# Kernel optimization log

Hardware: AMD Instinct MI355X
Metric: run time of the kernel (lower is better)

The kernel has to match this reference:

```python
import jax, jax.numpy as jnp
import numpy as np

# norse-default LIF/LI constants (RecNet overrides alpha=80, tau_mem_inv=100)
DT = 0.001
ALPHA = 80.0
TAU_SYN_INV = 200.0   # 1/5e-3 (default)
TAU_MEM_INV = 100.0   # 1/0.01 (passed explicitly)
V_TH, V_RESET, V_LEAK = 1.0, 0.0, 0.0

@jax.custom_vjp
def superspike(x):
    # heaviside forward, SuperSpike surrogate backward
    return (x > 0).astype(x.dtype)

def _ss_fwd(x):
    return (x > 0).astype(x.dtype), x

def _ss_bwd(x, g):
    return (g / (ALPHA * jnp.abs(x) + 1.0) ** 2,)

superspike.defvjp(_ss_fwd, _ss_bwd)

def setup_inputs() -> dict:
    key = jax.random.key(0)
    k1, k2, k3, k4 = jax.random.split(key, 4)
    T, B, F, H, O = 100, 512, 784, 512, 10
    x = jax.random.normal(k1, (T, B, 1, 28, 28), dtype=jnp.float32)
    w_in = jax.random.normal(k2, (H, F), dtype=jnp.float32) / np.sqrt(F)
    w_rec = jax.random.normal(k3, (H, H), dtype=jnp.float32) / np.sqrt(H)
    w_out = jax.random.normal(k4, (O, H), dtype=jnp.float32) / np.sqrt(H)
    return {"x": x, "w_in": w_in, "w_rec": w_rec, "w_out": w_out}

def reference(x, w_in, w_rec, w_out):
    T, B = x.shape[0], x.shape[1]
    Hd = w_in.shape[0]
    Od = w_out.shape[0]
    xf = x.reshape(T, B, -1)  # [T, B, F]

    z0 = jnp.zeros((B, Hd), x.dtype)
    lv0 = jnp.zeros((B, Od), x.dtype)
    init = (z0, z0, z0, lv0, lv0)  # (z, v, i, li_v, li_i)

    def step(carry, xt):
        z, v, i, lv, li = carry
        # LIF recurrent cell (norse lif_step)
        v_dec = v + DT * TAU_MEM_INV * ((V_LEAK - v) + i)
        i_dec = i - DT * TAU_SYN_INV * i
        z_new = superspike(v_dec - V_TH)
        v_new = (1.0 - z_new) * v_dec + z_new * V_RESET
        i_new = i_dec + xt @ w_in.T + z @ w_rec.T  # previous z for recurrence
        # readout linear (no bias)
        y = z_new @ w_out.T
        # LI cell (norse li_feed_forward_step): vo uses old current
        lv_new = lv + DT * TAU_MEM_INV * ((V_LEAK - lv) + li)
        li_new = li - DT * TAU_SYN_INV * li + y
        return (z_new, v_new, i_new, lv_new, li_new), lv_new

    _, voltages = jax.lax.scan(step, init, xf)
    return voltages  # [T, B, O]
```

## Files before the change

kernel.cpp:

```cpp
#include <hip/hip_runtime.h>


#define TT    100
#define BATCH 512
#define FDIM  784
#define HDIM  512
#define ODIM  10
#define NSTATE (BATCH * HDIM)

#define DTM 0.1
#define DTS 0.2

typedef double f64x4 __attribute__((ext_vector_type(4)));

__device__ __forceinline__ void h_maps(int H, int lane,
                                       int& am, int& ak, int& bn, int& bk,
                                       int dr[4], int dc[4]) {
  const int l15 = lane & 15, l4 = lane >> 4;
  const int lq = lane >> 2, l3 = lane & 3;
  if (H & 1) { am = lq;  ak = l3; } else { am = l15; ak = l4; }
  if (H & 2) { bn = lq;  bk = l3; } else { bn = l15; bk = l4; }
  const int dmode = H >> 2;
#pragma unroll
  for (int r = 0; r < 4; ++r) {
    const int rr = (dmode & 1) ? (l4 + (r << 2)) : ((l4 << 2) + r);
    if (dmode & 2) { dr[r] = l15; dc[r] = rr; }
    else           { dr[r] = rr;  dc[r] = l15; }
  }
}

__global__ __launch_bounds__(64) void probe_kernel(int* __restrict__ flag) {
  const int lane = threadIdx.x;
  int winner = -1;
  for (int H = 0; H < 16; ++H) {
    int am, ak, bn, bk, dr[4], dc[4];
    h_maps(H, lane, am, ak, bn, bk, dr, dc);
    bool ok = true;
#pragma unroll
    for (int s = 0; s < 2; ++s) {
      const int c0 = s ? 2 : 3, c1 = s ? 13 : 7, c2 = s ? 9 : 5, c3 = s ? 4 : 11;
      const double a = (double)(1 + c0 * am + c1 * ak);
      const double b = (double)(1 + c2 * bn + c3 * bk);
      f64x4 d = {0.0, 0.0, 0.0, 0.0};
      d = __builtin_amdgcn_mfma_f64_16x16x4f64(a, b, d, 0, 0, 0);
#pragma unroll
      for (int r = 0; r < 4; ++r) {
        double ref = 0.0;
#pragma unroll
        for (int k = 0; k < 4; ++k)
          ref += (double)((1 + c0 * dr[r] + c1 * k) * (1 + c2 * dc[r] + c3 * k));
        ok = ok && (d[r] == ref);
      }
    }
    if (__all(ok) && winner < 0) winner = H;
  }
  if (lane == 0) *flag = winner;
}

__global__ __launch_bounds__(256) void gemm_in_kernel(const float* __restrict__ A,
                                                      const float* __restrict__ B,
                                                      double* __restrict__ C,
                                                      const int* __restrict__ flag) {
  __shared__ __align__(16) double Al[4][16][16];
  __shared__ __align__(16) double Bl[4][16][16];
  const int tid  = threadIdx.x;
  const int lane = tid & 63;
  const int qm   = (tid >> 6) & 1;
  const int qn   = tid >> 7;
  const int n0 = blockIdx.x << 6;
  const int m0 = blockIdx.y << 6;
  const int srow = tid >> 2;
  const int skc  = (tid & 3) << 2;
  const int st = srow >> 4, sr = srow & 15;
  const int H = flag[0];

  const float* Arow = A + (size_t)(m0 + srow) * FDIM + skc;
  const float* Brow = B + (size_t)(n0 + srow) * FDIM + skc;

  if (H >= 0) {
    int am, ak, bn, bk, dr[4], dc[4];
    h_maps(H, lane, am, ak, bn, bk, dr, dc);
    f64x4 acc[2][2] = {};
    for (int kt = 0; kt < 49; ++kt) {
      __syncthreads();
      const float4 a4 = *(const float4*)(Arow + kt * 16);
      Al[st][skc + 0][sr] = (double)a4.x;
      Al[st][skc + 1][sr] = (double)a4.y;
      Al[st][skc + 2][sr] = (double)a4.z;
      Al[st][skc + 3][sr] = (double)a4.w;
      const float4 b4 = *(const float4*)(Brow + kt * 16);
      Bl[st][skc + 0][sr] = (double)b4.x;
      Bl[st][skc + 1][sr] = (double)b4.y;
      Bl[st][skc + 2][sr] = (double)b4.z;
      Bl[st][skc + 3][sr] = (double)b4.w;
      __syncthreads();
#pragma unroll
      for (int ks = 0; ks < 4; ++ks) {
        const double a0 = Al[(qm << 1) + 0][(ks << 2) + ak][am];
        const double a1 = Al[(qm << 1) + 1][(ks << 2) + ak][am];
        const double b0 = Bl[(qn << 1) + 0][(ks << 2) + bk][bn];
        const double b1 = Bl[(qn << 1) + 1][(ks << 2) + bk][bn];
        acc[0][0] = __builtin_amdgcn_mfma_f64_16x16x4f64(a0, b0, acc[0][0], 0, 0, 0);
        acc[0][1] = __builtin_amdgcn_mfma_f64_16x16x4f64(a0, b1, acc[0][1], 0, 0, 0);
        acc[1][0] = __builtin_amdgcn_mfma_f64_16x16x4f64(a1, b0, acc[1][0], 0, 0, 0);
        acc[1][1] = __builtin_amdgcn_mfma_f64_16x16x4f64(a1, b1, acc[1][1], 0, 0, 0);
      }
    }
#pragma unroll
    for (int i = 0; i < 2; ++i)
#pragma unroll
      for (int j = 0; j < 2; ++j)
#pragma unroll
        for (int r = 0; r < 4; ++r)
          C[(size_t)(m0 + (((qm << 1) + i) << 4) + dr[r]) * HDIM
            + n0 + (((qn << 1) + j) << 4) + dc[r]] = acc[i][j][r];
  } else {
    float* Asf = (float*)&Al[0][0][0];
    float* Bsf = (float*)&Bl[0][0][0];
    const int tn = tid & 15, tm = tid >> 4;
    const int lrow = tid >> 2, lkc = (tid & 3) << 2;
    double acc[4][4] = {};
    for (int kt = 0; kt < 49; ++kt) {
      __syncthreads();
      const float4 a = *(const float4*)(A + (size_t)(m0 + lrow) * FDIM + kt * 16 + lkc);
      Asf[(lkc + 0) * 68 + lrow] = a.x; Asf[(lkc + 1) * 68 + lrow] = a.y;
      Asf[(lkc + 2) * 68 + lrow] = a.z; Asf[(lkc + 3) * 68 + lrow] = a.w;
      const float4 b = *(const float4*)(B + (size_t)(n0 + lrow) * FDIM + kt * 16 + lkc);
      Bsf[(lkc + 0) * 68 + lrow] = b.x; Bsf[(lkc + 1) * 68 + lrow] = b.y;
      Bsf[(lkc + 2) * 68 + lrow] = b.z; Bsf[(lkc + 3) * 68 + lrow] = b.w;
      __syncthreads();
#pragma unroll
      for (int kk = 0; kk < 16; ++kk) {
        const float4 af = *(const float4*)&Asf[kk * 68 + (tm << 2)];
        const float4 bf = *(const float4*)&Bsf[kk * 68 + (tn << 2)];
        const double amv[4] = {(double)af.x, (double)af.y, (double)af.z, (double)af.w};
        const double bnv[4] = {(double)bf.x, (double)bf.y, (double)bf.z, (double)bf.w};
#pragma unroll
        for (int i = 0; i < 4; ++i)
#pragma unroll
          for (int j = 0; j < 4; ++j) acc[i][j] += amv[i] * bnv[j];
      }
    }
#pragma unroll
    for (int i = 0; i < 4; ++i) {
      double* crow = C + (size_t)(m0 + (tm << 2) + i) * HDIM + n0 + (tn << 2);
      *(double2*)(crow)     = make_double2(acc[i][0], acc[i][1]);
      *(double2*)(crow + 2) = make_double2(acc[i][2], acc[i][3]);
    }
  }
}

__global__ __launch_bounds__(256) void transpose_kernel(const float* __restrict__ src,
                                                        float* __restrict__ dst) {
  __shared__ float tile[32][33];
  const int bx = blockIdx.x & 15, by = blockIdx.x >> 4;
  const int tx = threadIdx.x & 31, ty = threadIdx.x >> 5;
  const int x = (bx << 5) + tx;
#pragma unroll
  for (int s = 0; s < 32; s += 8)
    tile[ty + s][tx] = src[(size_t)((by << 5) + ty + s) * HDIM + x];
  __syncthreads();
  const int xo = (by << 5) + tx;
#pragma unroll
  for (int s = 0; s < 32; s += 8)
    dst[(size_t)((bx << 5) + ty + s) * HDIM + xo] = tile[tx][ty + s];
}

__global__ __launch_bounds__(256) void wot_kernel(const float* __restrict__ w_out,
                                                  float* __restrict__ wot) {
  const int k = (blockIdx.x << 8) + threadIdx.x;
#pragma unroll
  for (int o = 0; o < ODIM; ++o) wot[(k << 4) + o] = w_out[(size_t)o * HDIM + k];
}

__global__ __launch_bounds__(256) void lif_kernel(const double* __restrict__ cin,
                                                  const float* __restrict__ wrt,
                                                  const float* __restrict__ wot,
                                                  float* __restrict__ out) {
  const int b = blockIdx.x;
  const int tid = threadIdx.x;
  const int h0 = tid, h1 = tid + 256;

  __shared__ unsigned long long masks[8];
  __shared__ int offs[9];
  __shared__ __align__(8) unsigned short list[528];
  __shared__ double ypart[256];

  if (tid == 0) offs[8] = 0;
  __syncthreads();

  double v0 = 0.0, v1 = 0.0, i0 = 0.0, i1 = 0.0;
  double lv = 0.0, li = 0.0;

  const double* cinb = cin + (size_t)b * HDIM;
  float* outb = out + (size_t)b * ODIM;

  for (int t = 0; t < TT; ++t) {
    const double vd0 = v0 + DTM * ((0.0 - v0) + i0);
    const double vd1 = v1 + DTM * ((0.0 - v1) + i1);
    const bool s0 = (vd0 - 1.0) > 0.0;
    const bool s1 = (vd1 - 1.0) > 0.0;
    v0 = s0 ? 0.0 : vd0;
    v1 = s1 ? 0.0 : vd1;
    i0 = i0 - DTS * i0;
    i1 = i1 - DTS * i1;

    const double c0 = cinb[(size_t)t * NSTATE + h0];
    const double c1 = cinb[(size_t)t * NSTATE + h1];

    {
      const int nf = offs[8];
      const int nfp = (nf + 3) & ~3;
      if (nfp > 0) {
        float A0[4], A1[4], B0[4] = {}, B1[4] = {};
#define LOADG(base, X0, X1)                                                   \
        do {                                                                  \
          const unsigned long long le = *(const unsigned long long*)&list[base]; \
          const int k0 = (int)(le & 0xffffu), k1 = (int)((le >> 16) & 0xffffu); \
          const int k2 = (int)((le >> 32) & 0xffffu), k3 = (int)(le >> 48);   \
          X0[0] = wrt[(k0 << 9) + h0]; X1[0] = wrt[(k0 << 9) + h1];           \
          X0[1] = wrt[(k1 << 9) + h0]; X1[1] = wrt[(k1 << 9) + h1];           \
          X0[2] = wrt[(k2 << 9) + h0]; X1[2] = wrt[(k2 << 9) + h1];           \
          X0[3] = wrt[(k3 << 9) + h0]; X1[3] = wrt[(k3 << 9) + h1];           \
        } while (0)
        LOADG(0, A0, A1);
        for (int g = 0; g < nfp; g += 4) {
          if (g + 4 < nfp) LOADG(g + 4, B0, B1);
          i0 += (double)A0[0]; i1 += (double)A1[0];
          i0 += (double)A0[1]; i1 += (double)A1[1];
          i0 += (double)A0[2]; i1 += (double)A1[2];
          i0 += (double)A0[3]; i1 += (double)A1[3];
#pragma unroll
          for (int j = 0; j < 4; ++j) { A0[j] = B0[j]; A1[j] = B1[j]; }
        }
#undef LOADG
      }
    }
    i0 += c0;
    i1 += c1;

    __syncthreads();

    {
      const unsigned long long m0 = __ballot(s0);
      const unsigned long long m1 = __ballot(s1);
      const int w = tid >> 6;
      if ((tid & 63) == 0) { masks[w] = m0; masks[4 + w] = m1; }
    }
    __syncthreads();
    if (tid == 0) {
      int r = 0;
#pragma unroll
      for (int q = 0; q < 8; ++q) { offs[q] = r; r += __popcll(masks[q]); }
      offs[8] = r;
    }
    __syncthreads();
    if (tid < 8) {
      unsigned long long m = masks[tid];
      int o = offs[tid];
      const int base = tid << 6;
      while (m) {
        list[o++] = (unsigned short)(base + __builtin_ctzll(m));
        m &= m - 1;
      }
    }
    if (tid < 4) list[offs[8] + tid] = 512;
    __syncthreads();

    {
      const int o = tid & 15, q = tid >> 4;
      const int nfc = offs[8];
      double yp = 0.0;
      int kk = q;
      if (kk < nfc) {
        float f = wot[((int)list[kk] << 4) + o];
        for (kk += 16; kk < nfc; kk += 16) {
          const float fn = wot[((int)list[kk] << 4) + o];
          yp += (double)f;
          f = fn;
        }
        yp += (double)f;
      }
      ypart[(o << 4) + q] = yp;
    }
    __syncthreads();
    if (tid < ODIM) {
      double y = 0.0;
      const double* yr = &ypart[tid << 4];
#pragma unroll
      for (int q = 0; q < 16; ++q) y += yr[q];
      const double lvn = lv + DTM * ((0.0 - lv) + li);
      li = (li - DTS * li) + y;
      lv = lvn;
      outb[(size_t)t * (BATCH * ODIM) + tid] = (float)lvn;
    }
  }
}

extern "C" void kernel_launch(void* const* d_in, const int* in_sizes, int n_in,
                              void* d_out, int out_size, void* d_ws, size_t ws_size,
                              hipStream_t stream) {
  const float* x     = (const float*)d_in[0];
  const float* w_in  = (const float*)d_in[1];
  const float* w_rec = (const float*)d_in[2];
  const float* w_out = (const float*)d_in[3];
  float* out = (float*)d_out;

  const size_t CIN = (size_t)TT * BATCH * HDIM;
  double* cin = (double*)d_ws;
  float* wrt = (float*)(cin + CIN);
  float* wot = wrt + 513 * 512;
  int* flag  = (int*)(wot + 513 * 16);

  const size_t aux_floats = 513ull * 512 + 513ull * 16;
  const size_t need_bytes = CIN * sizeof(double) + aux_floats * sizeof(float) + 16;
  if (ws_size < need_bytes) {
    hipMemsetAsync(d_out, 0x7F, (size_t)out_size * sizeof(float), stream);
    return;
  }

  hipMemsetAsync(wrt, 0, aux_floats * sizeof(float), stream);
  probe_kernel<<<1, 64, 0, stream>>>(flag);
  transpose_kernel<<<256, 256, 0, stream>>>(w_rec, wrt);
  wot_kernel<<<2, 256, 0, stream>>>(w_out, wot);
  gemm_in_kernel<<<dim3(8, 800), 256, 0, stream>>>(x, w_in, cin, flag);
  lif_kernel<<<BATCH, 256, 0, stream>>>(cin, wrt, wot, out);
}
```

Baseline: 1.192 ms.

## Enlarge input GEMM tile to 128x128 with double-buffered LDS prefetch

The fp64 MFMA input-projection GEMM now uses 128x128 output tiles per block, with a 4x4 fragment grid per wave instead of 2x2, so each loaded A/B element is reused more. It also double-buffers the LDS stage: the next k-slice is fetched into registers while MFMAs run on the current buffer, leaving one barrier per iteration. The aim is to cut global and LDS traffic per flop and to hide load latency. The cost is more accumulator registers (64 doubles per thread) and a smaller grid, which may lower occupancy. The fallback path loops over four 64x64 sub-tiles to match.

```diff
diff --git a/kernel.cpp b/kernel.cpp
--- a/kernel.cpp
+++ b/kernel.cpp
@@ -10,6 +10,8 @@
 
 #define DTM 0.1
 #define DTS 0.2
+
+#define LP 130
 
 typedef double f64x4 __attribute__((ext_vector_type(4)));
 
@@ -61,91 +63,125 @@
                                                       const float* __restrict__ B,
                                                       double* __restrict__ C,
                                                       const int* __restrict__ flag) {
-  __shared__ __align__(16) double Al[4][16][16];
-  __shared__ __align__(16) double Bl[4][16][16];
+  __shared__ __align__(16) double Al[2][16][LP];
+  __shared__ __align__(16) double Bl[2][16][LP];
   const int tid  = threadIdx.x;
   const int lane = tid & 63;
   const int qm   = (tid >> 6) & 1;
   const int qn   = tid >> 7;
-  const int n0 = blockIdx.x << 6;
-  const int m0 = blockIdx.y << 6;
-  const int srow = tid >> 2;
-  const int skc  = (tid & 3) << 2;
-  const int st = srow >> 4, sr = srow & 15;
+  const int n0 = blockIdx.x << 7;
+  const int m0 = blockIdx.y << 7;
   const int H = flag[0];
 
-  const float* Arow = A + (size_t)(m0 + srow) * FDIM + skc;
-  const float* Brow = B + (size_t)(n0 + srow) * FDIM + skc;
+  const int srow0 = tid >> 2;
+  const int skc   = (tid & 3) << 2;
+
+  const float* Arow0 = A + (size_t)(m0 + srow0) * FDIM + skc;
+  const float* Arow1 = Arow0 + (size_t)64 * FDIM;
+  const float* Brow0 = B + (size_t)(n0 + srow0) * FDIM + skc;
+  const float* Brow1 = Brow0 + (size_t)64 * FDIM;
 
   if (H >= 0) {
     int am, ak, bn, bk, dr[4], dc[4];
     h_maps(H, lane, am, ak, bn, bk, dr, dc);
-    f64x4 acc[2][2] = {};
+    f64x4 acc[4][4] = {};
+
+#define STAGE(bf, va0, va1, vb0, vb1)                                   \
+    do {                                                                \
+      _Pragma("unroll")                                                 \
+      for (int j = 0; j < 4; ++j) {                                     \
+        Al[bf][skc + j][srow0]      = (double)(&(va0).x)[j];            \
+        Al[bf][skc + j][srow0 + 64] = (double)(&(va1).x)[j];            \
+        Bl[bf][skc + j][srow0]      = (double)(&(vb0).x)[j];            \
+        Bl[bf][skc + j][srow0 + 64] = (double)(&(vb1).x)[j];            \
+      }                                                                 \
+    } while (0)
+
+    {
+      const float4 a0 = *(const float4*)(Arow0);
+      const float4 a1 = *(const float4*)(Arow1);
+      const float4 b0 = *(const float4*)(Brow0);
+      const float4 b1 = *(const float4*)(Brow1);
+      STAGE(0, a0, a1, b0, b1);
+    }
+    __syncthreads();
+
+    int cur = 0;
     for (int kt = 0; kt < 49; ++kt) {
+      float4 na0, na1, nb0, nb1;
+      if (kt < 48) {
+        na0 = *(const float4*)(Arow0 + (kt + 1) * 16);
+        na1 = *(const float4*)(Arow1 + (kt + 1) * 16);
+        nb0 = *(const float4*)(Brow0 + (kt + 1) * 16);
+        nb1 = *(const float4*)(Brow1 + (kt + 1) * 16);
+      }
+#pragma unroll
+      for (int ks = 0; ks < 4; ++ks) {
+        double fa[4], fb[4];
+#pragma unroll
+        for (int mf = 0; mf < 4; ++mf)
+          fa[mf] = Al[cur][(ks << 2) + ak][(qm << 6) + (mf << 4) + am];
+#pragma unroll
+        for (int nf = 0; nf < 4; ++nf)
+          fb[nf] = Bl[cur][(ks << 2) + bk][(qn << 6) + (nf << 4) + bn];
+#pragma unroll
+        for (int mf = 0; mf < 4; ++mf)
+#pragma unroll
+          for (int nf = 0; nf < 4; ++nf)
+            acc[mf][nf] = __builtin_amdgcn_mfma_f64_16x16x4f64(fa[mf], fb[nf],
+                                                               acc[mf][nf], 0, 0, 0);
+      }
+      if (kt < 48) STAGE(cur ^ 1, na0, na1, nb0, nb1);
       __syncthreads();
-      const float4 a4 = *(const float4*)(Arow + kt * 16);
-      Al[st][skc + 0][sr] = (double)a4.x;
-      Al[st][skc + 1][sr] = (double)a4.y;
-      Al[st][skc + 2][sr] = (double)a4.z;
-      Al[st][skc + 3][sr] = (double)a4.w;
-      const float4 b4 = *(const float4*)(Brow + kt * 16);
-      Bl[st][skc + 0][sr] = (double)b4.x;
-      Bl[st][skc + 1][sr] = (double)b4.y;
-      Bl[st][skc + 2][sr] = (double)b4.z;
-      Bl[st][skc + 3][sr] = (double)b4.w;
-      __syncthreads();
-#pragma unroll
-      for (int ks = 0; ks < 4; ++ks) {
-        const double a0 = Al[(qm << 1) + 0][(ks << 2) + ak][am];
-        const double a1 = Al[(qm << 1) + 1][(ks << 2) + ak][am];
-        const double b0 = Bl[(qn << 1) + 0][(ks << 2) + bk][bn];
-        const double b1 = Bl[(qn << 1) + 1][(ks << 2) + bk][bn];
-        acc[0][0] = __builtin_amdgcn_mfma_f64_16x16x4f64(a0, b0, acc[0][0], 0, 0, 0);
-        acc[0][1] = __builtin_amdgcn_mfma_f64_16x16x4f64(a0, b1, acc[0][1], 0, 0, 0);
-        acc[1][0] = __builtin_amdgcn_mfma_f64_16x16x4f64(a1, b0, acc[1][0], 0, 0, 0);
-        acc[1][1] = __builtin_amdgcn_mfma_f64_16x16x4f64(a1, b1, acc[1][1], 0, 0, 0);
-      }
-    }
-#pragma unroll
-    for (int i = 0; i < 2; ++i)
-#pragma unroll
-      for (int j = 0; j < 2; ++j)
+      cur ^= 1;
+    }
+#undef STAGE
+
+#pragma unroll
+    for (int mf = 0; mf < 4; ++mf)
+#pragma unroll
+      for (int nf = 0; nf < 4; ++nf)
 #pragma unroll
         for (int r = 0; r < 4; ++r)
-          C[(size_t)(m0 + (((qm << 1) + i) << 4) + dr[r]) * HDIM
-            + n0 + (((qn << 1) + j) << 4) + dc[r]] = acc[i][j][r];
+          C[(size_t)(m0 + (qm << 6) + (mf << 4) + dr[r]) * HDIM
+            + n0 + (qn << 6) + (nf << 4) + dc[r]] = acc[mf][nf][r];
   } else {
     float* Asf = (float*)&Al[0][0][0];
     float* Bsf = (float*)&Bl[0][0][0];
     const int tn = tid & 15, tm = tid >> 4;
     const int lrow = tid >> 2, lkc = (tid & 3) << 2;
-    double acc[4][4] = {};
-    for (int kt = 0; kt < 49; ++kt) {
+    for (int sub = 0; sub < 4; ++sub) {
+      const int sm0 = m0 + ((sub & 1) << 6);
+      const int sn0 = n0 + ((sub >> 1) << 6);
+      double acc[4][4] = {};
+      for (int kt = 0; kt < 49; ++kt) {
+        __syncthreads();
+        const float4 a = *(const float4*)(A + (size_t)(sm0 + lrow) * FDIM + kt * 16 + lkc);
+        Asf[(lkc + 0) * 68 + lrow] = a.x; Asf[(lkc + 1) * 68 + lrow] = a.y;
+        Asf[(lkc + 2) * 68 + lrow] = a.z; Asf[(lkc + 3) * 68 + lrow] = a.w;
+        const float4 b = *(const float4*)(B + (size_t)(sn0 + lrow) * FDIM + kt * 16 + lkc);
+        Bsf[(lkc + 0) * 68 + lrow] = b.x; Bsf[(lkc + 1) * 68 + lrow] = b.y;
+        Bsf[(lkc + 2) * 68 + lrow] = b.z; Bsf[(lkc + 3) * 68 + lrow] = b.w;
+        __syncthreads();
+#pragma unroll
+        for (int kk = 0; kk < 16; ++kk) {
+          const float4 af = *(const float4*)&Asf[kk * 68 + (tm << 2)];
+          const float4 bf = *(const float4*)&Bsf[kk * 68 + (tn << 2)];
+          const double amv[4] = {(double)af.x, (double)af.y, (double)af.z, (double)af.w};
+          const double bnv[4] = {(double)bf.x, (double)bf.y, (double)bf.z, (double)bf.w};
+#pragma unroll
+          for (int i = 0; i < 4; ++i)
+#pragma unroll
+            for (int j = 0; j < 4; ++j) acc[i][j] += amv[i] * bnv[j];
+        }
+      }
+#pragma unroll
+      for (int i = 0; i < 4; ++i) {
+        double* crow = C + (size_t)(sm0 + (tm << 2) + i) * HDIM + sn0 + (tn << 2);
+        *(double2*)(crow)     = make_double2(acc[i][0], acc[i][1]);
+        *(double2*)(crow + 2) = make_double2(acc[i][2], acc[i][3]);
+      }
       __syncthreads();
-      const float4 a = *(const float4*)(A + (size_t)(m0 + lrow) * FDIM + kt * 16 + lkc);
-      Asf[(lkc + 0) * 68 + lrow] = a.x; Asf[(lkc + 1) * 68 + lrow] = a.y;
-      Asf[(lkc + 2) * 68 + lrow] = a.z; Asf[(lkc + 3) * 68 + lrow] = a.w;
-      const float4 b = *(const float4*)(B + (size_t)(n0 + lrow) * FDIM + kt * 16 + lkc);
-      Bsf[(lkc + 0) * 68 + lrow] = b.x; Bsf[(lkc + 1) * 68 + lrow] = b.y;
-      Bsf[(lkc + 2) * 68 + lrow] = b.z; Bsf[(lkc + 3) * 68 + lrow] = b.w;
-      __syncthreads();
-#pragma unroll
-      for (int kk = 0; kk < 16; ++kk) {
-        const float4 af = *(const float4*)&Asf[kk * 68 + (tm << 2)];
-        const float4 bf = *(const float4*)&Bsf[kk * 68 + (tn << 2)];
-        const double amv[4] = {(double)af.x, (double)af.y, (double)af.z, (double)af.w};
-        const double bnv[4] = {(double)bf.x, (double)bf.y, (double)bf.z, (double)bf.w};
-#pragma unroll
-        for (int i = 0; i < 4; ++i)
-#pragma unroll
-          for (int j = 0; j < 4; ++j) acc[i][j] += amv[i] * bnv[j];
-      }
-    }
-#pragma unroll
-    for (int i = 0; i < 4; ++i) {
-      double* crow = C + (size_t)(m0 + (tm << 2) + i) * HDIM + n0 + (tn << 2);
-      *(double2*)(crow)     = make_double2(acc[i][0], acc[i][1]);
-      *(double2*)(crow + 2) = make_double2(acc[i][2], acc[i][3]);
     }
   }
 }
@@ -323,6 +359,6 @@
   probe_kernel<<<1, 64, 0, stream>>>(flag);
   transpose_kernel<<<256, 256, 0, stream>>>(w_rec, wrt);
   wot_kernel<<<2, 256, 0, stream>>>(w_out, wot);
-  gemm_in_kernel<<<dim3(8, 800), 256, 0, stream>>>(x, w_in, cin, flag);
+  gemm_in_kernel<<<dim3(4, 400), 256, 0, stream>>>(x, w_in, cin, flag);
   lif_kernel<<<BATCH, 256, 0, stream>>>(cin, wrt, wot, out);
 }
```

After: 1.320 ms. 10.8% more time.

## Split input GEMM rows between FP64 MFMA blocks and VALU FMA blocks

Applied to the files above, without the earlier changes.

The input-projection GEMM now runs as a 1D grid where each period of 37 blocks mixes 24 MFMA-tiled blocks (64x64 tiles, first 24576 rows) and 13 VALU-FMA blocks (128x64 tiles, remaining 26624 rows). The aim is to use the FP64 matrix cores and the vector ALUs at the same time, so the GEMM is no longer limited by matrix-core throughput alone. Interleaving the two block types keeps both kinds resident on each CU. The risk is an imbalance between the two paths, and the larger shared-memory footprint may reduce occupancy.

```diff
diff --git a/kernel.cpp b/kernel.cpp
--- a/kernel.cpp
+++ b/kernel.cpp
@@ -10,6 +10,10 @@
 
 #define DTM 0.1
 #define DTS 0.2
+
+#define M_MFMA_BLKS 3072
+#define M_VALU_BLKS 1664
+#define PERIOD 37
 
 typedef double f64x4 __attribute__((ext_vector_type(4)));
 
@@ -61,25 +65,29 @@
                                                       const float* __restrict__ B,
                                                       double* __restrict__ C,
                                                       const int* __restrict__ flag) {
-  __shared__ __align__(16) double Al[4][16][16];
-  __shared__ __align__(16) double Bl[4][16][16];
-  const int tid  = threadIdx.x;
-  const int lane = tid & 63;
-  const int qm   = (tid >> 6) & 1;
-  const int qn   = tid >> 7;
-  const int n0 = blockIdx.x << 6;
-  const int m0 = blockIdx.y << 6;
-  const int srow = tid >> 2;
-  const int skc  = (tid & 3) << 2;
-  const int st = srow >> 4, sr = srow & 15;
+  __shared__ __align__(16) char smem[25088];
+  const int tid = threadIdx.x;
+  const int id = blockIdx.x;
+  const int p = id / PERIOD, r = id % PERIOD;
+  const bool is_mfma_blk = (r < 24);
   const int H = flag[0];
 
-  const float* Arow = A + (size_t)(m0 + srow) * FDIM + skc;
-  const float* Brow = B + (size_t)(n0 + srow) * FDIM + skc;
-
-  if (H >= 0) {
+  if (is_mfma_blk && H >= 0) {
+    const int mb = p * 24 + r;
+    const int n0 = (mb & 7) << 6;
+    const int m0 = (mb >> 3) << 6;
+    double (*Al)[16][16] = (double(*)[16][16])smem;
+    double (*Bl)[16][16] = (double(*)[16][16])(smem + 8192);
+    const int lane = tid & 63;
+    const int qm = (tid >> 6) & 1;
+    const int qn = tid >> 7;
+    const int srow = tid >> 2;
+    const int skc  = (tid & 3) << 2;
+    const int st = srow >> 4, sr = srow & 15;
     int am, ak, bn, bk, dr[4], dc[4];
     h_maps(H, lane, am, ak, bn, bk, dr, dc);
+    const float* Arow = A + (size_t)(m0 + srow) * FDIM + skc;
+    const float* Brow = B + (size_t)(n0 + srow) * FDIM + skc;
     f64x4 acc[2][2] = {};
     for (int kt = 0; kt < 49; ++kt) {
       __syncthreads();
@@ -111,12 +119,15 @@
 #pragma unroll
       for (int j = 0; j < 2; ++j)
 #pragma unroll
-        for (int r = 0; r < 4; ++r)
-          C[(size_t)(m0 + (((qm << 1) + i) << 4) + dr[r]) * HDIM
-            + n0 + (((qn << 1) + j) << 4) + dc[r]] = acc[i][j][r];
-  } else {
-    float* Asf = (float*)&Al[0][0][0];
-    float* Bsf = (float*)&Bl[0][0][0];
+        for (int rr = 0; rr < 4; ++rr)
+          C[(size_t)(m0 + (((qm << 1) + i) << 4) + dr[rr]) * HDIM
+            + n0 + (((qn << 1) + j) << 4) + dc[rr]] = acc[i][j][rr];
+  } else if (is_mfma_blk) {
+    const int mb = p * 24 + r;
+    const int n0 = (mb & 7) << 6;
+    const int m0 = (mb >> 3) << 6;
+    float* Asf = (float*)smem;
+    float* Bsf = (float*)(smem + 4352);
     const int tn = tid & 15, tm = tid >> 4;
     const int lrow = tid >> 2, lkc = (tid & 3) << 2;
     double acc[4][4] = {};
@@ -144,6 +155,55 @@
 #pragma unroll
     for (int i = 0; i < 4; ++i) {
       double* crow = C + (size_t)(m0 + (tm << 2) + i) * HDIM + n0 + (tn << 2);
+      *(double2*)(crow)     = make_double2(acc[i][0], acc[i][1]);
+      *(double2*)(crow + 2) = make_double2(acc[i][2], acc[i][3]);
+    }
+  } else {
+    const int vb = p * 13 + (r - 24);
+    const int n0 = (vb & 7) << 6;
+    const int m0 = 24576 + ((vb >> 3) << 7);
+    double (*As)[130] = (double(*)[130])smem;
+    double (*Bs)[66]  = (double(*)[66])(smem + 16640);
+    const int tn = tid & 15;
+    const int tm = tid >> 4;
+    double acc[8][4] = {};
+    for (int kt = 0; kt < 49; ++kt) {
+      __syncthreads();
+#pragma unroll
+      for (int s = 0; s < 2; ++s) {
+        const int idx = tid + (s << 8);
+        const int row = idx >> 2;
+        const int kc  = (idx & 3) << 2;
+        const float4 a = *(const float4*)(A + (size_t)(m0 + row) * FDIM + kt * 16 + kc);
+        As[kc + 0][row] = (double)a.x; As[kc + 1][row] = (double)a.y;
+        As[kc + 2][row] = (double)a.z; As[kc + 3][row] = (double)a.w;
+      }
+      {
+        const int row = tid >> 2;
+        const int kc  = (tid & 3) << 2;
+        const float4 b = *(const float4*)(B + (size_t)(n0 + row) * FDIM + kt * 16 + kc);
+        Bs[kc + 0][row] = (double)b.x; Bs[kc + 1][row] = (double)b.y;
+        Bs[kc + 2][row] = (double)b.z; Bs[kc + 3][row] = (double)b.w;
+      }
+      __syncthreads();
+#pragma unroll
+      for (int kk = 0; kk < 16; ++kk) {
+        double av[8], bv[4];
+        *(double2*)&av[0] = *(const double2*)&As[kk][(tm << 3) + 0];
+        *(double2*)&av[2] = *(const double2*)&As[kk][(tm << 3) + 2];
+        *(double2*)&av[4] = *(const double2*)&As[kk][(tm << 3) + 4];
+        *(double2*)&av[6] = *(const double2*)&As[kk][(tm << 3) + 6];
+        *(double2*)&bv[0] = *(const double2*)&Bs[kk][(tn << 2) + 0];
+        *(double2*)&bv[2] = *(const double2*)&Bs[kk][(tn << 2) + 2];
+#pragma unroll
+        for (int i = 0; i < 8; ++i)
+#pragma unroll
+          for (int j = 0; j < 4; ++j) acc[i][j] += av[i] * bv[j];
+      }
+    }
+#pragma unroll
+    for (int i = 0; i < 8; ++i) {
+      double* crow = C + (size_t)(m0 + (tm << 3) + i) * HDIM + n0 + (tn << 2);
       *(double2*)(crow)     = make_double2(acc[i][0], acc[i][1]);
       *(double2*)(crow + 2) = make_double2(acc[i][2], acc[i][3]);
     }
@@ -249,10 +309,10 @@
     }
     __syncthreads();
     if (tid == 0) {
-      int r = 0;
-#pragma unroll
-      for (int q = 0; q < 8; ++q) { offs[q] = r; r += __popcll(masks[q]); }
-      offs[8] = r;
+      int rr = 0;
+#pragma unroll
+      for (int q = 0; q < 8; ++q) { offs[q] = rr; rr += __popcll(masks[q]); }
+      offs[8] = rr;
     }
     __syncthreads();
     if (tid < 8) {
@@ -323,6 +383,6 @@
   probe_kernel<<<1, 64, 0, stream>>>(flag);
   transpose_kernel<<<256, 256, 0, stream>>>(w_rec, wrt);
   wot_kernel<<<2, 256, 0, stream>>>(w_out, wot);
-  gemm_in_kernel<<<dim3(8, 800), 256, 0, stream>>>(x, w_in, cin, flag);
+  gemm_in_kernel<<<M_MFMA_BLKS + M_VALU_BLKS, 256, 0, stream>>>(x, w_in, cin, flag);
   lif_kernel<<<BATCH, 256, 0, stream>>>(cin, wrt, wot, out);
 }
```

After: 1.313 ms. +10.2%, slower.
